# Kernel optimization log

Measured on AMD Instinct MI355X. Metric: run time of the kernel, lower is better.

## Reference

```python
import jax, jax.numpy as jnp
import numpy as np

N, E, HN, K = 4096, 8192, 1024, 8
NF, EF = 128, 64
NH = [256, 256]
EH = [64, 64]
EMB = NH[-1] + len(EH)  # 258
BN_EPS = 1e-5


def setup_inputs() -> dict:
    key = jax.random.key(0)
    ks = jax.random.split(key, 16)

    def nrm(k, shape, fan):
        return jax.random.normal(k, shape, jnp.float32) / np.float32(np.sqrt(fan))

    return {
        "X_n": jax.random.normal(ks[0], (N, NF), jnp.float32),
        "X_e": jax.random.normal(ks[1], (E, EF), jnp.float32),
        # row-normalized-ish adjacency and scaled Laplacian to keep activations bounded
        "A_tilde": jax.random.uniform(ks[2], (N, N), jnp.float32) / np.float32(N),
        "L1_tilde": jax.random.normal(ks[3], (E, E), jnp.float32) / np.float32(np.sqrt(E)),
        "B1": jax.random.normal(ks[4], (N, E), jnp.float32) / np.float32(np.sqrt(E)),
        # GNN params (Linear stores weight as [out, in])
        "gnn_W1": nrm(ks[5], (NH[0], NF), NF), "gnn_b1": jnp.zeros((NH[0],), jnp.float32),
        "gnn_W2": nrm(ks[6], (NH[1], NH[0]), NH[0]), "gnn_b2": jnp.zeros((NH[1],), jnp.float32),
        # HoSC layer 1: in=EF, out=EH[0]
        "hosc_W1": nrm(ks[7], (EH[0], EF), EF), "hosc_b1": jnp.zeros((EH[0],), jnp.float32),
        "bn1_g": jnp.ones((EH[0],), jnp.float32), "bn1_b": jnp.zeros((EH[0],), jnp.float32),
        # HoSC layer 2: in=1 (after channel-max), out=EH[1]
        "hosc_W2": nrm(ks[8], (EH[1], 1), 1), "hosc_b2": jnp.zeros((EH[1],), jnp.float32),
        "bn2_g": jnp.ones((EH[1],), jnp.float32), "bn2_b": jnp.zeros((EH[1],), jnp.float32),
        # heads
        "node_W": nrm(ks[9], (1, EMB), EMB), "node_b": jnp.zeros((1,), jnp.float32),
        "edge_W": nrm(ks[10], (1, len(EH)), len(EH)), "edge_b": jnp.zeros((1,), jnp.float32),
        "hyper_W": nrm(ks[11], (1, EMB), EMB), "hyper_b": jnp.zeros((1,), jnp.float32),
        "hyperedges": jax.random.randint(ks[12], (HN, K), 0, N, jnp.int64),
    }


def _bn(x, g, b):
    # training-mode BatchNorm1d: biased batch statistics over rows
    m = jnp.mean(x, axis=0)
    v = jnp.var(x, axis=0)
    return g * (x - m) / jnp.sqrt(v + BN_EPS) + b


def _hosc_layer(Z, L1, W, bias, g, b):
    Zt = Z @ W.T + bias            # [E, out]
    Zc = L1 @ Zt                   # [E, out]
    Zp = jax.nn.relu(_bn(Zc, g, b))
    return jnp.max(Zp, axis=1, keepdims=True)  # [E, 1]


def reference(X_n, X_e, A_tilde, L1_tilde, B1,
              gnn_W1, gnn_b1, gnn_W2, gnn_b2,
              hosc_W1, hosc_b1, bn1_g, bn1_b,
              hosc_W2, hosc_b2, bn2_g, bn2_b,
              node_W, node_b, edge_W, edge_b, hyper_W, hyper_b,
              hyperedges):
    # --- GNN over nodes ---
    H = jax.nn.relu((A_tilde @ X_n) @ gnn_W1.T + gnn_b1)   # [N, 256]
    H_n = jax.nn.relu((A_tilde @ H) @ gnn_W2.T + gnn_b2)   # [N, 256]

    # --- HoSC over edges ---
    Z1 = _hosc_layer(X_e, L1_tilde, hosc_W1, hosc_b1, bn1_g, bn1_b)  # [E, 1]
    Z2 = _hosc_layer(Z1, L1_tilde, hosc_W2, hosc_b2, bn2_g, bn2_b)   # [E, 1]
    Z_H = jnp.concatenate([Z1, Z2], axis=1)                 # [E, 2]

    # --- fuse edge info into nodes ---
    H_e = B1 @ Z_H                                          # [N, 2]
    Hcat = jnp.concatenate([H_n, H_e], axis=1)              # [N, 258]

    node_prob = jax.nn.sigmoid(Hcat @ node_W.T + node_b).squeeze(-1)  # [N]
    edge_prob = jax.nn.sigmoid(Z_H @ edge_W.T + edge_b).squeeze(-1)   # [E]

    # vectorized hyperedge gather-mean-linear-sigmoid (fixed-size hyperedges)
    hfeat = Hcat[hyperedges].mean(axis=1)                   # [HN, 258]
    hyperedge_prob = jax.nn.sigmoid(hfeat @ hyper_W.T + hyper_b)  # [HN, 1]

    return node_prob, edge_prob, hyperedge_prob, Hcat
```

## Files before the change

kernel.cpp:

```cpp
#include <hip/hip_runtime.h>
#include <hip/hip_bf16.h>

using f32x4  = __attribute__((ext_vector_type(4))) float;
using u32x4  = __attribute__((ext_vector_type(4))) unsigned int;
using bf16x8 = __attribute__((ext_vector_type(8))) short;

__device__ __forceinline__ ushort f2bf(float x) {
    union { __hip_bfloat16 h; ushort u; } cv;
    cv.h = __float2bfloat16(x);
    return cv.u;
}
__device__ __forceinline__ unsigned pk2(float lo, float hi) {
    return (unsigned)f2bf(lo) | ((unsigned)f2bf(hi) << 16);
}
__device__ __forceinline__ float sigmoidf_(float x) { return 1.f / (1.f + expf(-x)); }

template<int NSUM, bool A_BF16, bool ABR, bool SPLIT, bool RELU, bool BF16_OUT, bool HAS_BIAS>
__device__ __forceinline__ void gemm_body(
    ushort* As, ushort* Bs,
    const void* __restrict__ Avoid, const ushort* __restrict__ B,
    const float* __restrict__ abias, const float* __restrict__ bias,
    float* __restrict__ Cf, ushort* __restrict__ Cb,
    int M, int N, int K, int ldc, int kPerChunk, long pStride,
    int bx, int by, int bz)
{
    const int tid  = threadIdx.x;
    const int lane = tid & 63;
    const int wid  = tid >> 6;
    const int wr   = wid >> 1, wc = wid & 1;
    const int g    = lane >> 4, lr = lane & 15;
    const long m0  = (long)bx * 128;
    const int  n0  = by * 64;

    int kbeg = 0, kend = K;
    if (SPLIT) { kbeg = bz * kPerChunk; kend = kbeg + kPerChunk; if (kend > K) kend = K; }

    const int bkr = tid & 31;
    const int bcb = tid >> 5;

    const float*  Af = (const float*)Avoid;
    const ushort* Ab = (const ushort*)Avoid;

    f32x4 pa[4];
    u32x4 pab[2];
    u32x4 pb;

    auto loadT = [&](int k0) {
        if (A_BF16) {
#pragma unroll
            for (int i = 0; i < 2; i++) {
                int s = tid + 256 * i; int row = s >> 2, c8 = s & 3;
                pab[i] = *(const u32x4*)(Ab + (m0 + row) * (long)K + k0 + c8 * 8);
            }
        } else {
#pragma unroll
            for (int i = 0; i < 4; i++) {
                int s = tid + 256 * i; int row = s >> 3, c4 = s & 7;
                const float* base = Af + (m0 + row) * (long)K + k0 + c4 * 4;
                f32x4 v = *(const f32x4*)base;
                if (NSUM > 0) {
#pragma unroll
                    for (int z = 1; z < NSUM; z++) v += *(const f32x4*)(base + z * pStride);
                }
                if (ABR) {
                    f32x4 bq = *(const f32x4*)(abias + k0 + c4 * 4);
                    v.x = fmaxf(v.x + bq.x, 0.f);
                    v.y = fmaxf(v.y + bq.y, 0.f);
                    v.z = fmaxf(v.z + bq.z, 0.f);
                    v.w = fmaxf(v.w + bq.w, 0.f);
                }
                pa[i] = v;
            }
        }
        pb = *(const u32x4*)(B + (long)(k0 + bkr) * N + n0 + bcb * 8);
    };
    auto storeT = [&]() {
        if (A_BF16) {
#pragma unroll
            for (int i = 0; i < 2; i++) {
                int s = tid + 256 * i; int row = s >> 2, c8 = s & 3;
                *(u32x4*)(&As[row * 40 + c8 * 8]) = pab[i];
            }
        } else {
#pragma unroll
            for (int i = 0; i < 4; i++) {
                int s = tid + 256 * i; int row = s >> 3, c4 = s & 7;
                ushort4 w;
                w.x = f2bf(pa[i].x); w.y = f2bf(pa[i].y);
                w.z = f2bf(pa[i].z); w.w = f2bf(pa[i].w);
                *(ushort4*)(&As[row * 40 + c4 * 4]) = w;
            }
        }
        const ushort* p8 = (const ushort*)&pb;
#pragma unroll
        for (int j = 0; j < 8; j++) Bs[(bcb * 8 + j) * 40 + bkr] = p8[j];
    };

    f32x4 acc[4][2] = {};

    const int nk = (kend - kbeg) >> 5;
    loadT(kbeg);
    for (int t = 0; t < nk; ++t) {
        storeT();
        __syncthreads();
        if (t + 1 < nk) loadT(kbeg + ((t + 1) << 5));
        bf16x8 af[4], bfr[2];
#pragma unroll
        for (int fm = 0; fm < 4; fm++)
            af[fm] = *(const bf16x8*)(&As[(wr * 64 + fm * 16 + lr) * 40 + g * 8]);
#pragma unroll
        for (int fn = 0; fn < 2; fn++)
            bfr[fn] = *(const bf16x8*)(&Bs[(wc * 32 + fn * 16 + lr) * 40 + g * 8]);
#pragma unroll
        for (int fm = 0; fm < 4; fm++)
#pragma unroll
            for (int fn = 0; fn < 2; fn++)
                acc[fm][fn] = __builtin_amdgcn_mfma_f32_16x16x32_bf16(af[fm], bfr[fn], acc[fm][fn], 0, 0, 0);
        __syncthreads();
    }

    if (SPLIT) {
        float* P = Cf + (long)bz * M * N;
#pragma unroll
        for (int fm = 0; fm < 4; fm++)
#pragma unroll
            for (int fn = 0; fn < 2; fn++)
#pragma unroll
                for (int rr = 0; rr < 4; rr++) {
                    long row = m0 + wr * 64 + fm * 16 + g * 4 + rr;
                    int  col = n0 + wc * 32 + fn * 16 + lr;
                    P[row * N + col] = acc[fm][fn][rr];
                }
    } else {
#pragma unroll
        for (int fm = 0; fm < 4; fm++)
#pragma unroll
            for (int fn = 0; fn < 2; fn++)
#pragma unroll
                for (int rr = 0; rr < 4; rr++) {
                    long row = m0 + wr * 64 + fm * 16 + g * 4 + rr;
                    int  col = n0 + wc * 32 + fn * 16 + lr;
                    float v = acc[fm][fn][rr];
                    if (HAS_BIAS) v += bias[col];
                    if (RELU) v = fmaxf(v, 0.f);
                    if (BF16_OUT) Cb[row * ldc + col] = f2bf(v);
                    else          Cf[row * ldc + col] = v;
                }
    }
}

__global__ __launch_bounds__(256)
void prep_k(const float* __restrict__ A, ushort* __restrict__ Abf,
            const float* __restrict__ Xn, const float* __restrict__ W1, ushort* __restrict__ T1,
            const float* __restrict__ Xe, const float* __restrict__ Wh,
            const float* __restrict__ hb, ushort* __restrict__ Zt1,
            const float* __restrict__ W2, ushort* __restrict__ W2t,
            float* __restrict__ stats)
{
    __shared__ float xs[1024];
    int b = blockIdx.x, t = threadIdx.x;
    if (b < 8192) {
        long j = (long)b * 256 + t;
        f32x4 v0 = ((const f32x4*)A)[2 * j];
        f32x4 v1 = ((const f32x4*)A)[2 * j + 1];
        u32x4 w;
        w.x = pk2(v0.x, v0.y); w.y = pk2(v0.z, v0.w);
        w.z = pk2(v1.x, v1.y); w.w = pk2(v1.z, v1.w);
        ((u32x4*)Abf)[j] = w;
    } else if (b < 8704) {
        int r0 = (b - 8192) * 8;
        for (int idx = t; idx < 1024; idx += 256) xs[idx] = Xn[(long)r0 * 128 + idx];
        __syncthreads();
        float acc[8] = {};
        const float* wrow = W1 + (long)t * 128;
        for (int i = 0; i < 128; i++) {
            float w = wrow[i];
#pragma unroll
            for (int r = 0; r < 8; r++) acc[r] += xs[r * 128 + i] * w;
        }
#pragma unroll
        for (int r = 0; r < 8; r++) T1[(long)(r0 + r) * 256 + t] = f2bf(acc[r]);
    } else if (b < 10752) {
        int row = (b - 8704) * 4 + (t >> 6);
        int o   = t & 63;
        const float* xr = Xe + (long)row * 64;
        const float* wr = Wh + (long)o * 64;
        float acc = hb[o];
#pragma unroll 8
        for (int i = 0; i < 64; i++) acc += xr[i] * wr[i];
        Zt1[(long)row * 64 + o] = f2bf(acc);
    } else if (b < 11008) {
        int j = (b - 10752) * 256 + t;
        int i = j >> 8, o = j & 255;
        W2t[j] = f2bf(W2[o * 256 + i]);
    } else {
        if (t < 256) stats[t] = 0.f;
    }
}

__device__ __forceinline__ void bnred_body(int b, const float* __restrict__ P,
                                           float* __restrict__ Zc,
                                           float* __restrict__ pstats,
                                           float* __restrict__ gsum, float* __restrict__ gsq,
                                           unsigned* __restrict__ ctr)
{
    const long MN = 8192 * 64;
    int t = threadIdx.x;
    int c = t & 63, rg = t >> 6;
    float sx = 0.f, sq = 0.f;
    int base = b * 32 + rg;
#pragma unroll 4
    for (int i = 0; i < 8; i++) {
        long idx = (long)(base + 4 * i) * 64 + c;
        float x = 0.f;
#pragma unroll
        for (int z = 0; z < 8; z++) x += P[idx + z * MN];
        Zc[idx] = x;
        sx += x; sq += x * x;
    }
    __shared__ float ls[256], lq[256];
    ls[t] = sx; lq[t] = sq;
    __syncthreads();
    if (t < 64) {
        float a = ls[t] + ls[t + 64] + ls[t + 128] + ls[t + 192];
        float q = lq[t] + lq[t + 64] + lq[t + 128] + lq[t + 192];
        pstats[b * 128 + t]      = a;
        pstats[b * 128 + 64 + t] = q;
    }
    __threadfence();
    __syncthreads();
    __shared__ unsigned lastflag;
    if (t == 0) {
        unsigned old = atomicAdd(ctr, 1u);
        lastflag = (old == 255u);
    }
    __syncthreads();
    if (lastflag) {
        __threadfence();
        if (t < 128) {
            float a = 0.f;
            for (int bb = 0; bb < 256; bb++) a += pstats[bb * 128 + t];
            if (t < 64) gsum[t] = a;
            else        gsq[t - 64] = a;
        }
    }
}

__device__ __forceinline__ void z1_body(int b, const float* __restrict__ Zc,
                                        const float* __restrict__ gsum, const float* __restrict__ gsq,
                                        const float* __restrict__ g, const float* __restrict__ bb,
                                        float* __restrict__ Z1)
{
    int w = threadIdx.x >> 6, lane = threadIdx.x & 63;
    int row = b * 4 + w;
    const float inv = 1.f / 8192.f;
    float m = gsum[lane] * inv;
    float v = gsq[lane] * inv - m * m;
    float x = Zc[row * 64 + lane];
    float y = fmaxf(g[lane] * (x - m) * rsqrtf(v + 1e-5f) + bb[lane], 0.f);
#pragma unroll
    for (int o = 32; o > 0; o >>= 1) y = fmaxf(y, __shfl_xor(y, o));
    if (lane == 0) Z1[row] = y;
}

__device__ __forceinline__ void pass2_body(int row, const float* __restrict__ L1,
                                           const float* __restrict__ Z1,
                                           float* __restrict__ s, float* __restrict__ r)
{
    int t = threadIdx.x;
    int l = t & 63, w = t >> 6;
    const f32x4* rp = (const f32x4*)(L1 + (long)row * 8192);
    const f32x4* z4 = (const f32x4*)Z1;
    float as = 0.f, ar = 0.f;
#pragma unroll 4
    for (int k = 0; k < 8; k++) {
        f32x4 v = rp[t + 256 * k];
        f32x4 z = z4[t + 256 * k];
        as += v.x * z.x + v.y * z.y + v.z * z.z + v.w * z.w;
        ar += v.x + v.y + v.z + v.w;
    }
#pragma unroll
    for (int o = 32; o > 0; o >>= 1) { as += __shfl_xor(as, o); ar += __shfl_xor(ar, o); }
    __shared__ float sw[4], rw[4];
    if (l == 0) { sw[w] = as; rw[w] = ar; }
    __syncthreads();
    if (t == 0) {
        s[row] = sw[0] + sw[1] + sw[2] + sw[3];
        r[row] = rw[0] + rw[1] + rw[2] + rw[3];
    }
}

__device__ __forceinline__ void hcatred_body(int b, const float* __restrict__ P,
                                             const float* __restrict__ b2, float* __restrict__ hcat)
{
    const long MNq = (long)4096 * 256 / 4;
    int j = b * 256 + threadIdx.x;
    int row = j >> 6, c4 = (j & 63) * 4;
    const f32x4* Q = (const f32x4*)P;
    f32x4 v = Q[j] + Q[j + MNq] + Q[j + 2 * MNq] + Q[j + 3 * MNq];
    f32x4 bq = *(const f32x4*)(b2 + c4);
    float* dst = hcat + (long)row * 258 + c4;
    float2 lo = { fmaxf(v.x + bq.x, 0.f), fmaxf(v.y + bq.y, 0.f) };
    float2 hi = { fmaxf(v.z + bq.z, 0.f), fmaxf(v.w + bq.w, 0.f) };
    *(float2*)dst = lo;
    *(float2*)(dst + 2) = hi;
}

__global__ __launch_bounds__(256)
void dual_a_k(const float* __restrict__ L1, const ushort* __restrict__ Zt1, float* __restrict__ Pa,
              const ushort* __restrict__ Abf, const ushort* __restrict__ T1, float* __restrict__ Pb)
{
    __shared__ ushort As[128 * 40];
    __shared__ ushort Bs[64 * 40];
    int bid = blockIdx.x;
    if (bid < 512) {
        gemm_body<0, false, false, true, false, false, false>(
            As, Bs, L1, Zt1, nullptr, nullptr, Pa, nullptr,
            8192, 64, 8192, 64, 1024, 0, bid & 63, 0, bid >> 6);
    } else {
        int b = bid - 512;
        gemm_body<0, true, false, true, false, false, false>(
            As, Bs, Abf, T1, nullptr, nullptr, Pb, nullptr,
            4096, 256, 4096, 256, 1024, 0, b & 31, (b >> 5) & 3, b >> 7);
    }
}

__global__ __launch_bounds__(256)
void dual_b_k(const float* __restrict__ Pb, const float* __restrict__ gb1,
              const ushort* __restrict__ W2t, ushort* __restrict__ T2,
              const float* __restrict__ Pa, float* __restrict__ Zc1,
              float* __restrict__ pstats,
              float* __restrict__ gsum, float* __restrict__ gsq, unsigned* __restrict__ ctr)
{
    __shared__ ushort As[128 * 40];
    __shared__ ushort Bs[64 * 40];
    int bid = blockIdx.x;
    if (bid < 128) {
        gemm_body<4, false, true, false, false, true, false>(
            As, Bs, Pb, W2t, gb1, nullptr, nullptr, T2,
            4096, 256, 256, 256, 0, (long)4096 * 256, bid & 31, bid >> 5, 0);
    } else {
        bnred_body(bid - 128, Pa, Zc1, pstats, gsum, gsq, ctr);
    }
}

__global__ __launch_bounds__(256)
void dual_c_k(const ushort* __restrict__ Abf, const ushort* __restrict__ T2, float* __restrict__ Pa,
              const float* __restrict__ Zc1, const float* __restrict__ gsum,
              const float* __restrict__ gsq, const float* __restrict__ bn1g,
              const float* __restrict__ bn1b, float* __restrict__ Z1)
{
    __shared__ ushort As[128 * 40];
    __shared__ ushort Bs[64 * 40];
    int bid = blockIdx.x;
    if (bid < 512) {
        gemm_body<0, true, false, true, false, false, false>(
            As, Bs, Abf, T2, nullptr, nullptr, Pa, nullptr,
            4096, 256, 4096, 256, 1024, 0, bid & 31, (bid >> 5) & 3, bid >> 7);
    } else {
        z1_body(bid - 512, Zc1, gsum, gsq, bn1g, bn1b, Z1);
    }
}

__global__ __launch_bounds__(256)
void dual_d_k(const float* __restrict__ Pa, const float* __restrict__ gb2, float* __restrict__ hcat,
              const float* __restrict__ L1, const float* __restrict__ Z1,
              float* __restrict__ s, float* __restrict__ r)
{
    int bid = blockIdx.x;
    if (bid < 1024) hcatred_body(bid, Pa, gb2, hcat);
    else            pass2_body(bid - 1024, L1, Z1, s, r);
}

__global__ __launch_bounds__(1024) void stats2_k(const float* __restrict__ s, const float* __restrict__ r,
                                                 float* __restrict__ S5)
{
    int t = threadIdx.x, l = t & 63, w = t >> 6;
    float Ss = 0, Sr = 0, Sss = 0, Srr = 0, Ssr = 0;
    for (int i = t; i < 8192; i += 1024) {
        float sv = s[i], rv = r[i];
        Ss += sv; Sr += rv; Sss += sv * sv; Srr += rv * rv; Ssr += sv * rv;
    }
#pragma unroll
    for (int o = 32; o > 0; o >>= 1) {
        Ss += __shfl_xor(Ss, o); Sr += __shfl_xor(Sr, o);
        Sss += __shfl_xor(Sss, o); Srr += __shfl_xor(Srr, o); Ssr += __shfl_xor(Ssr, o);
    }
    __shared__ float buf[16][5];
    if (l == 0) { buf[w][0] = Ss; buf[w][1] = Sr; buf[w][2] = Sss; buf[w][3] = Srr; buf[w][4] = Ssr; }
    __syncthreads();
    if (t < 5) {
        float a = 0.f;
#pragma unroll
        for (int i = 0; i < 16; i++) a += buf[i][t];
        S5[t] = a;
    }
}

__global__ __launch_bounds__(256) void z2_edge_k(const float* __restrict__ s, const float* __restrict__ r,
                                                 const float* __restrict__ S,
                                                 const float* __restrict__ W2, const float* __restrict__ b2,
                                                 const float* __restrict__ g2, const float* __restrict__ bb2,
                                                 const float* __restrict__ eW, const float* __restrict__ eb,
                                                 const float* __restrict__ Z1,
                                                 float* __restrict__ Z2, float* __restrict__ edge_out)
{
    int w = threadIdx.x >> 6, lane = threadIdx.x & 63;
    int row = blockIdx.x * 4 + w;
    const float inv = 1.f / 8192.f;
    float ms = S[0] * inv, mr = S[1] * inv;
    float vs = S[2] * inv - ms * ms;
    float vr = S[3] * inv - mr * mr;
    float cv = S[4] * inv - ms * mr;
    float w2 = W2[lane], bz = b2[lane];
    float mc = w2 * ms + bz * mr;
    float vc = w2 * w2 * vs + 2.f * w2 * bz * cv + bz * bz * vr;
    float x  = w2 * s[row] + bz * r[row];
    float y  = fmaxf(g2[lane] * (x - mc) * rsqrtf(vc + 1e-5f) + bb2[lane], 0.f);
#pragma unroll
    for (int o = 32; o > 0; o >>= 1) y = fmaxf(y, __shfl_xor(y, o));
    if (lane == 0) {
        Z2[row] = y;
        float e = Z1[row] * eW[0] + y * eW[1] + eb[0];
        edge_out[row] = sigmoidf_(e);
    }
}

__global__ __launch_bounds__(256) void he_node_k(const float* __restrict__ B1, const float* __restrict__ Z1,
                                                 const float* __restrict__ Z2, float* __restrict__ hcat,
                                                 const float* __restrict__ nW, const float* __restrict__ nb,
                                                 float* __restrict__ node_out)
{
    int n = blockIdx.x, t = threadIdx.x;
    int l = t & 63, w = t >> 6;
    const f32x4* rp  = (const f32x4*)(B1 + (long)n * 8192);
    const f32x4* z1v = (const f32x4*)Z1;
    const f32x4* z2v = (const f32x4*)Z2;
    float a1 = 0.f, a2 = 0.f;
#pragma unroll 4
    for (int k = 0; k < 8; k++) {
        f32x4 v = rp[t + 256 * k];
        f32x4 p = z1v[t + 256 * k];
        f32x4 q = z2v[t + 256 * k];
        a1 += v.x * p.x + v.y * p.y + v.z * p.z + v.w * p.w;
        a2 += v.x * q.x + v.y * q.y + v.z * q.z + v.w * q.w;
    }
    float d = hcat[(long)n * 258 + t] * nW[t];
#pragma unroll
    for (int o = 32; o > 0; o >>= 1) {
        a1 += __shfl_xor(a1, o); a2 += __shfl_xor(a2, o); d += __shfl_xor(d, o);
    }
    __shared__ float s1[4], s2[4], s3[4];
    if (l == 0) { s1[w] = a1; s2[w] = a2; s3[w] = d; }
    __syncthreads();
    if (t == 0) {
        float A1 = s1[0] + s1[1] + s1[2] + s1[3];
        float A2 = s2[0] + s2[1] + s2[2] + s2[3];
        float D  = s3[0] + s3[1] + s3[2] + s3[3];
        hcat[(long)n * 258 + 256] = A1;
        hcat[(long)n * 258 + 257] = A2;
        node_out[n] = sigmoidf_(D + A1 * nW[256] + A2 * nW[257] + nb[0]);
    }
}

__global__ __launch_bounds__(256) void hyper_k(const void* __restrict__ he_idx,
                                               const float* __restrict__ hcat,
                                               const float* __restrict__ hW, const float* __restrict__ hb,
                                               float* __restrict__ out)
{
    int w = threadIdx.x >> 6, lane = threadIdx.x & 63;
    int h = blockIdx.x * 4 + w;
    const unsigned int* u = (const unsigned int*)he_idx;
    unsigned int odd = u[2 * lane + 1];
    bool is64 = __all(odd == 0u);
    float acc = 0.f;
    for (int k = 0; k < 8; k++) {
        int idx;
        if (is64) idx = (int)((const long long*)he_idx)[h * 8 + k];
        else      idx = ((const int*)he_idx)[h * 8 + k];
        const float* hr = hcat + (long)idx * 258;
        for (int d = lane; d < 258; d += 64) acc += hr[d] * hW[d];
    }
    acc *= 0.125f;
#pragma unroll
    for (int o = 32; o > 0; o >>= 1) acc += __shfl_xor(acc, o);
    if (lane == 0) out[h] = sigmoidf_(acc + hb[0]);
}

extern "C" void kernel_launch(void* const* d_in, const int* in_sizes, int n_in,
                              void* d_out, int out_size, void* d_ws, size_t ws_size,
                              hipStream_t stream)
{
    const float* X_n  = (const float*)d_in[0];
    const float* X_e  = (const float*)d_in[1];
    const float* A_t  = (const float*)d_in[2];
    const float* L1   = (const float*)d_in[3];
    const float* B1   = (const float*)d_in[4];
    const float* gW1  = (const float*)d_in[5];
    const float* gb1  = (const float*)d_in[6];
    const float* gW2  = (const float*)d_in[7];
    const float* gb2  = (const float*)d_in[8];
    const float* hW1  = (const float*)d_in[9];
    const float* hb1  = (const float*)d_in[10];
    const float* bn1g = (const float*)d_in[11];
    const float* bn1b = (const float*)d_in[12];
    const float* hW2  = (const float*)d_in[13];
    const float* hb2  = (const float*)d_in[14];
    const float* bn2g = (const float*)d_in[15];
    const float* bn2b = (const float*)d_in[16];
    const float* nW   = (const float*)d_in[17];
    const float* nb   = (const float*)d_in[18];
    const float* eW   = (const float*)d_in[19];
    const float* ebb  = (const float*)d_in[20];
    const float* yW   = (const float*)d_in[21];
    const float* yb   = (const float*)d_in[22];
    const void*  he   = d_in[23];

    float* out       = (float*)d_out;
    float* out_node  = out;
    float* out_edge  = out + 4096;
    float* out_hyper = out + 12288;
    float* hcat      = out + 13312;

    size_t off = 0;
    auto alloc = [&](size_t bytes) {
        void* p = (char*)d_ws + off;
        off = (off + bytes + 255) & ~(size_t)255;
        return p;
    };
    ushort* Abf    = (ushort*)alloc((size_t)4096 * 4096 * 2);
    ushort* T1     = (ushort*)alloc(4096 * 256 * 2);
    ushort* T2     = (ushort*)alloc(4096 * 256 * 2);
    ushort* Zt1    = (ushort*)alloc(8192 * 64 * 2);
    ushort* W2t    = (ushort*)alloc(256 * 256 * 2);
    float*  Zc1    = (float*)alloc(8192 * 64 * 4);
    float*  stats  = (float*)alloc(256 * 4);
    float*  gsum   = stats;
    float*  gsq    = stats + 64;
    float*  S5     = stats + 128;
    unsigned* ctr  = (unsigned*)(stats + 192);
    float*  pstats = (float*)alloc(256 * 128 * 4);
    float*  Z1     = (float*)alloc(8192 * 4);
    float*  Z2     = (float*)alloc(8192 * 4);
    float*  sbuf   = (float*)alloc(8192 * 4);
    float*  rbuf   = (float*)alloc(8192 * 4);
    float*  Pa     = (float*)alloc((size_t)8192 * 64 * 8 * 4);
    float*  Pb     = (float*)alloc((size_t)4096 * 256 * 4 * 4);

    prep_k<<<11009, 256, 0, stream>>>(A_t, Abf, X_n, gW1, T1, X_e, hW1, hb1, Zt1,
                                      gW2, W2t, stats);

    dual_a_k<<<1024, 256, 0, stream>>>(L1, Zt1, Pa, Abf, T1, Pb);

    dual_b_k<<<384, 256, 0, stream>>>(Pb, gb1, W2t, T2, Pa, Zc1, pstats, gsum, gsq, ctr);

    dual_c_k<<<2560, 256, 0, stream>>>(Abf, T2, Pa, Zc1, gsum, gsq, bn1g, bn1b, Z1);

    dual_d_k<<<9216, 256, 0, stream>>>(Pa, gb2, hcat, L1, Z1, sbuf, rbuf);

    stats2_k<<<1, 1024, 0, stream>>>(sbuf, rbuf, S5);

    z2_edge_k<<<2048, 256, 0, stream>>>(sbuf, rbuf, S5, hW2, hb2, bn2g, bn2b,
                                        eW, ebb, Z1, Z2, out_edge);

    he_node_k<<<4096, 256, 0, stream>>>(B1, Z1, Z2, hcat, nW, nb, out_node);

    hyper_k<<<256, 256, 0, stream>>>(he, hcat, yW, yb, out_hyper);
}
```

Baseline: 311.3 us.

## Drop stats2 kernel, use atomics for BN stats, coarsen pass2 and node blocks

Replaces the last-block pstats reduction in the BN1 statistics with direct float atomicAdd into gsum/gsq. Removes the single-block stats2 kernel by having every z2_edge block recompute the global sums over s and r redundantly. The pass2 blocks in dual_d and the he_node blocks are each made to process four rows per block, which cuts grid sizes. This saves one launch and some block-scheduling overhead, at the cost of nondeterministic atomic ordering and 2048 blocks each re-reading the full 8192-entry s/r arrays.

```diff
diff --git a/kernel.cpp b/kernel.cpp
--- a/kernel.cpp
+++ b/kernel.cpp
@@ -200,9 +200,7 @@
 
 __device__ __forceinline__ void bnred_body(int b, const float* __restrict__ P,
                                            float* __restrict__ Zc,
-                                           float* __restrict__ pstats,
-                                           float* __restrict__ gsum, float* __restrict__ gsq,
-                                           unsigned* __restrict__ ctr)
+                                           float* __restrict__ gsum, float* __restrict__ gsq)
 {
     const long MN = 8192 * 64;
     int t = threadIdx.x;
@@ -224,25 +222,8 @@
     if (t < 64) {
         float a = ls[t] + ls[t + 64] + ls[t + 128] + ls[t + 192];
         float q = lq[t] + lq[t + 64] + lq[t + 128] + lq[t + 192];
-        pstats[b * 128 + t]      = a;
-        pstats[b * 128 + 64 + t] = q;
-    }
-    __threadfence();
-    __syncthreads();
-    __shared__ unsigned lastflag;
-    if (t == 0) {
-        unsigned old = atomicAdd(ctr, 1u);
-        lastflag = (old == 255u);
-    }
-    __syncthreads();
-    if (lastflag) {
-        __threadfence();
-        if (t < 128) {
-            float a = 0.f;
-            for (int bb = 0; bb < 256; bb++) a += pstats[bb * 128 + t];
-            if (t < 64) gsum[t] = a;
-            else        gsq[t - 64] = a;
-        }
+        atomicAdd(&gsum[t], a);
+        atomicAdd(&gsq[t], q);
     }
 }
 
@@ -288,6 +269,7 @@
         s[row] = sw[0] + sw[1] + sw[2] + sw[3];
         r[row] = rw[0] + rw[1] + rw[2] + rw[3];
     }
+    __syncthreads();
 }
 
 __device__ __forceinline__ void hcatred_body(int b, const float* __restrict__ P,
@@ -329,8 +311,7 @@
 void dual_b_k(const float* __restrict__ Pb, const float* __restrict__ gb1,
               const ushort* __restrict__ W2t, ushort* __restrict__ T2,
               const float* __restrict__ Pa, float* __restrict__ Zc1,
-              float* __restrict__ pstats,
-              float* __restrict__ gsum, float* __restrict__ gsq, unsigned* __restrict__ ctr)
+              float* __restrict__ gsum, float* __restrict__ gsq)
 {
     __shared__ ushort As[128 * 40];
     __shared__ ushort Bs[64 * 40];
@@ -340,7 +321,7 @@
             As, Bs, Pb, W2t, gb1, nullptr, nullptr, T2,
             4096, 256, 256, 256, 0, (long)4096 * 256, bid & 31, bid >> 5, 0);
     } else {
-        bnred_body(bid - 128, Pa, Zc1, pstats, gsum, gsq, ctr);
+        bnred_body(bid - 128, Pa, Zc1, gsum, gsq);
     }
 }
 
@@ -368,16 +349,27 @@
               float* __restrict__ s, float* __restrict__ r)
 {
     int bid = blockIdx.x;
-    if (bid < 1024) hcatred_body(bid, Pa, gb2, hcat);
-    else            pass2_body(bid - 1024, L1, Z1, s, r);
-}
-
-__global__ __launch_bounds__(1024) void stats2_k(const float* __restrict__ s, const float* __restrict__ r,
-                                                 float* __restrict__ S5)
+    if (bid < 1024) {
+        hcatred_body(bid, Pa, gb2, hcat);
+    } else {
+        int pb = bid - 1024;
+#pragma unroll
+        for (int i = 0; i < 4; i++)
+            pass2_body(i * 2048 + pb, L1, Z1, s, r);
+    }
+}
+
+__global__ __launch_bounds__(256)
+void z2_edge_k(const float* __restrict__ s, const float* __restrict__ r,
+               const float* __restrict__ W2, const float* __restrict__ b2,
+               const float* __restrict__ g2, const float* __restrict__ bb2,
+               const float* __restrict__ eW, const float* __restrict__ eb,
+               const float* __restrict__ Z1,
+               float* __restrict__ Z2, float* __restrict__ edge_out)
 {
     int t = threadIdx.x, l = t & 63, w = t >> 6;
     float Ss = 0, Sr = 0, Sss = 0, Srr = 0, Ssr = 0;
-    for (int i = t; i < 8192; i += 1024) {
+    for (int i = t; i < 8192; i += 256) {
         float sv = s[i], rv = r[i];
         Ss += sv; Sr += rv; Sss += sv * sv; Srr += rv * rv; Ssr += sv * rv;
     }
@@ -386,40 +378,29 @@
         Ss += __shfl_xor(Ss, o); Sr += __shfl_xor(Sr, o);
         Sss += __shfl_xor(Sss, o); Srr += __shfl_xor(Srr, o); Ssr += __shfl_xor(Ssr, o);
     }
-    __shared__ float buf[16][5];
+    __shared__ float buf[4][5];
     if (l == 0) { buf[w][0] = Ss; buf[w][1] = Sr; buf[w][2] = Sss; buf[w][3] = Srr; buf[w][4] = Ssr; }
     __syncthreads();
-    if (t < 5) {
-        float a = 0.f;
-#pragma unroll
-        for (int i = 0; i < 16; i++) a += buf[i][t];
-        S5[t] = a;
-    }
-}
-
-__global__ __launch_bounds__(256) void z2_edge_k(const float* __restrict__ s, const float* __restrict__ r,
-                                                 const float* __restrict__ S,
-                                                 const float* __restrict__ W2, const float* __restrict__ b2,
-                                                 const float* __restrict__ g2, const float* __restrict__ bb2,
-                                                 const float* __restrict__ eW, const float* __restrict__ eb,
-                                                 const float* __restrict__ Z1,
-                                                 float* __restrict__ Z2, float* __restrict__ edge_out)
-{
-    int w = threadIdx.x >> 6, lane = threadIdx.x & 63;
+    float S0 = buf[0][0] + buf[1][0] + buf[2][0] + buf[3][0];
+    float S1 = buf[0][1] + buf[1][1] + buf[2][1] + buf[3][1];
+    float S2 = buf[0][2] + buf[1][2] + buf[2][2] + buf[3][2];
+    float S3 = buf[0][3] + buf[1][3] + buf[2][3] + buf[3][3];
+    float S4 = buf[0][4] + buf[1][4] + buf[2][4] + buf[3][4];
+
     int row = blockIdx.x * 4 + w;
     const float inv = 1.f / 8192.f;
-    float ms = S[0] * inv, mr = S[1] * inv;
-    float vs = S[2] * inv - ms * ms;
-    float vr = S[3] * inv - mr * mr;
-    float cv = S[4] * inv - ms * mr;
-    float w2 = W2[lane], bz = b2[lane];
+    float ms = S0 * inv, mr = S1 * inv;
+    float vs = S2 * inv - ms * ms;
+    float vr = S3 * inv - mr * mr;
+    float cv = S4 * inv - ms * mr;
+    float w2 = W2[l], bz = b2[l];
     float mc = w2 * ms + bz * mr;
     float vc = w2 * w2 * vs + 2.f * w2 * bz * cv + bz * bz * vr;
     float x  = w2 * s[row] + bz * r[row];
-    float y  = fmaxf(g2[lane] * (x - mc) * rsqrtf(vc + 1e-5f) + bb2[lane], 0.f);
+    float y  = fmaxf(g2[l] * (x - mc) * rsqrtf(vc + 1e-5f) + bb2[l], 0.f);
 #pragma unroll
     for (int o = 32; o > 0; o >>= 1) y = fmaxf(y, __shfl_xor(y, o));
-    if (lane == 0) {
+    if (l == 0) {
         Z2[row] = y;
         float e = Z1[row] * eW[0] + y * eW[1] + eb[0];
         edge_out[row] = sigmoidf_(e);
@@ -431,35 +412,40 @@
                                                  const float* __restrict__ nW, const float* __restrict__ nb,
                                                  float* __restrict__ node_out)
 {
-    int n = blockIdx.x, t = threadIdx.x;
+    int t = threadIdx.x;
     int l = t & 63, w = t >> 6;
-    const f32x4* rp  = (const f32x4*)(B1 + (long)n * 8192);
+    __shared__ float s1[4], s2[4], s3[4];
     const f32x4* z1v = (const f32x4*)Z1;
     const f32x4* z2v = (const f32x4*)Z2;
-    float a1 = 0.f, a2 = 0.f;
+#pragma unroll
+    for (int i = 0; i < 4; i++) {
+        int n = i * 1024 + blockIdx.x;
+        const f32x4* rp = (const f32x4*)(B1 + (long)n * 8192);
+        float a1 = 0.f, a2 = 0.f;
 #pragma unroll 4
-    for (int k = 0; k < 8; k++) {
-        f32x4 v = rp[t + 256 * k];
-        f32x4 p = z1v[t + 256 * k];
-        f32x4 q = z2v[t + 256 * k];
-        a1 += v.x * p.x + v.y * p.y + v.z * p.z + v.w * p.w;
-        a2 += v.x * q.x + v.y * q.y + v.z * q.z + v.w * q.w;
-    }
-    float d = hcat[(long)n * 258 + t] * nW[t];
-#pragma unroll
-    for (int o = 32; o > 0; o >>= 1) {
-        a1 += __shfl_xor(a1, o); a2 += __shfl_xor(a2, o); d += __shfl_xor(d, o);
-    }
-    __shared__ float s1[4], s2[4], s3[4];
-    if (l == 0) { s1[w] = a1; s2[w] = a2; s3[w] = d; }
-    __syncthreads();
-    if (t == 0) {
-        float A1 = s1[0] + s1[1] + s1[2] + s1[3];
-        float A2 = s2[0] + s2[1] + s2[2] + s2[3];
-        float D  = s3[0] + s3[1] + s3[2] + s3[3];
-        hcat[(long)n * 258 + 256] = A1;
-        hcat[(long)n * 258 + 257] = A2;
-        node_out[n] = sigmoidf_(D + A1 * nW[256] + A2 * nW[257] + nb[0]);
+        for (int k = 0; k < 8; k++) {
+            f32x4 v = rp[t + 256 * k];
+            f32x4 p = z1v[t + 256 * k];
+            f32x4 q = z2v[t + 256 * k];
+            a1 += v.x * p.x + v.y * p.y + v.z * p.z + v.w * p.w;
+            a2 += v.x * q.x + v.y * q.y + v.z * q.z + v.w * q.w;
+        }
+        float d = hcat[(long)n * 258 + t] * nW[t];
+#pragma unroll
+        for (int o = 32; o > 0; o >>= 1) {
+            a1 += __shfl_xor(a1, o); a2 += __shfl_xor(a2, o); d += __shfl_xor(d, o);
+        }
+        if (l == 0) { s1[w] = a1; s2[w] = a2; s3[w] = d; }
+        __syncthreads();
+        if (t == 0) {
+            float A1 = s1[0] + s1[1] + s1[2] + s1[3];
+            float A2 = s2[0] + s2[1] + s2[2] + s2[3];
+            float D  = s3[0] + s3[1] + s3[2] + s3[3];
+            hcat[(long)n * 258 + 256] = A1;
+            hcat[(long)n * 258 + 257] = A2;
+            node_out[n] = sigmoidf_(D + A1 * nW[256] + A2 * nW[257] + nb[0]);
+        }
+        __syncthreads();
     }
 }
 
@@ -537,9 +523,6 @@
     float*  stats  = (float*)alloc(256 * 4);
     float*  gsum   = stats;
     float*  gsq    = stats + 64;
-    float*  S5     = stats + 128;
-    unsigned* ctr  = (unsigned*)(stats + 192);
-    float*  pstats = (float*)alloc(256 * 128 * 4);
     float*  Z1     = (float*)alloc(8192 * 4);
     float*  Z2     = (float*)alloc(8192 * 4);
     float*  sbuf   = (float*)alloc(8192 * 4);
@@ -552,18 +535,16 @@
 
     dual_a_k<<<1024, 256, 0, stream>>>(L1, Zt1, Pa, Abf, T1, Pb);
 
-    dual_b_k<<<384, 256, 0, stream>>>(Pb, gb1, W2t, T2, Pa, Zc1, pstats, gsum, gsq, ctr);
+    dual_b_k<<<384, 256, 0, stream>>>(Pb, gb1, W2t, T2, Pa, Zc1, gsum, gsq);
 
     dual_c_k<<<2560, 256, 0, stream>>>(Abf, T2, Pa, Zc1, gsum, gsq, bn1g, bn1b, Z1);
 
-    dual_d_k<<<9216, 256, 0, stream>>>(Pa, gb2, hcat, L1, Z1, sbuf, rbuf);
-
-    stats2_k<<<1, 1024, 0, stream>>>(sbuf, rbuf, S5);
-
-    z2_edge_k<<<2048, 256, 0, stream>>>(sbuf, rbuf, S5, hW2, hb2, bn2g, bn2b,
+    dual_d_k<<<3072, 256, 0, stream>>>(Pa, gb2, hcat, L1, Z1, sbuf, rbuf);
+
+    z2_edge_k<<<2048, 256, 0, stream>>>(sbuf, rbuf, hW2, hb2, bn2g, bn2b,
                                         eW, ebb, Z1, Z2, out_edge);
 
-    he_node_k<<<4096, 256, 0, stream>>>(B1, Z1, Z2, hcat, nW, nb, out_node);
+    he_node_k<<<1024, 256, 0, stream>>>(B1, Z1, Z2, hcat, nW, nb, out_node);
 
     hyper_k<<<256, 256, 0, stream>>>(he, hcat, yW, yb, out_hyper);
 }
```

Measured after the change: 301.7 us. 1.03x faster.
